# Optimization experiments

Measured on AMD Instinct MI355X. Metric: run time of the kernel, lower is better.

Reference implementation:

```python
import jax, jax.numpy as jnp
import numpy as np
from jax import lax

B, CIN, H, W = 16, 96, 112, 112
C1, C2 = CIN * 2, CIN * 4          # 192, 384 (t1=(2,2))
SQ = 24                            # make_divisible(96//4, 4)
EPS = 1e-5


def _conv(x, w, stride, pad, groups):
    return lax.conv_general_dilated(
        x, w, window_strides=stride, padding=pad,
        feature_group_count=groups,
        dimension_numbers=("NCHW", "OIHW", "NCHW"))


def _bn(x, g, b, m, v):
    scale = (g / jnp.sqrt(v + EPS))[None, :, None, None]
    return (x - m[None, :, None, None]) * scale + b[None, :, None, None]


def _shuffle(x, groups):
    b, c, h, w = x.shape
    return x.reshape(b, groups, c // groups, h, w).transpose(0, 2, 1, 3, 4).reshape(b, c, h, w)


# DYShiftMax channel permutation for g=1: rotate channels left by 1
_DY_IDX = np.roll(np.arange(CIN), -1)


def setup_inputs() -> dict:
    key = jax.random.key(0)
    ks = jax.random.split(key, 16)
    f32 = jnp.float32
    d = {}
    d["x"] = jax.random.normal(ks[0], (B, CIN, H, W), f32)
    # depthwise (k,1) conv, groups=CIN, multiplier 2
    d["w_dw1"] = jax.random.normal(ks[1], (C1, 1, 3, 1), f32) * 0.2
    d["bn1_g"] = jax.random.uniform(ks[2], (C1,), f32, 0.5, 1.5)
    d["bn1_b"] = jax.random.normal(ks[3], (C1,), f32) * 0.1
    d["bn1_m"] = jax.random.normal(ks[4], (C1,), f32) * 0.1
    d["bn1_v"] = jax.random.uniform(ks[5], (C1,), f32, 0.5, 1.5)
    # depthwise (1,k) conv, groups=C1, multiplier 2
    d["w_dw2"] = jax.random.normal(ks[6], (C2, 1, 1, 3), f32) * 0.2
    d["bn2_g"] = jax.random.uniform(ks[7], (C2,), f32, 0.5, 1.5)
    d["bn2_b"] = jax.random.normal(ks[8], (C2,), f32) * 0.1
    d["bn2_m"] = jax.random.normal(ks[9], (C2,), f32) * 0.1
    d["bn2_v"] = jax.random.uniform(ks[10], (C2,), f32, 0.5, 1.5)
    # 1x1 pointwise conv 384 -> 96 (ConvModule, bias-free conv + BN, identity act)
    d["w_pw"] = jax.random.normal(ks[11], (CIN, C2, 1, 1), f32) * (1.0 / np.sqrt(C2))
    d["bn3_g"] = jax.random.uniform(ks[12], (CIN,), f32, 0.5, 1.5)
    d["bn3_b"] = jax.random.normal(ks[13], (CIN,), f32) * 0.1
    d["bn3_m"] = jax.random.normal(ks[14], (CIN,), f32) * 0.1
    d["bn3_v"] = jax.random.uniform(ks[15], (CIN,), f32, 0.5, 1.5)
    # DYShiftMax squeeze-excite FC: CIN -> SQ -> 2*CIN (exp=2)
    k2 = jax.random.split(jax.random.fold_in(key, 1), 4)
    d["fc1_w"] = jax.random.normal(k2[0], (SQ, CIN), f32) * (1.0 / np.sqrt(CIN))
    d["fc1_b"] = jax.random.normal(k2[1], (SQ,), f32) * 0.1
    d["fc2_w"] = jax.random.normal(k2[2], (2 * CIN, SQ), f32) * (1.0 / np.sqrt(SQ))
    d["fc2_b"] = jax.random.normal(k2[3], (2 * CIN,), f32) * 0.1
    return d


def reference(x, w_dw1, bn1_g, bn1_b, bn1_m, bn1_v,
              w_dw2, bn2_g, bn2_b, bn2_m, bn2_v,
              w_pw, bn3_g, bn3_b, bn3_m, bn3_v,
              fc1_w, fc1_b, fc2_w, fc2_b):
    # DepthSpatialSepConv: depthwise (3,1) then depthwise (1,3), each + BN
    h = _conv(x, w_dw1, (1, 1), ((1, 1), (0, 0)), groups=CIN)
    h = _bn(h, bn1_g, bn1_b, bn1_m, bn1_v)
    h = _conv(h, w_dw2, (1, 1), ((0, 0), (1, 1)), groups=C1)
    h = _bn(h, bn2_g, bn2_b, bn2_m, bn2_v)
    # ReLU6 (y2 == 0)
    h = jnp.clip(h, 0.0, 6.0)
    # ChannelShuffle(6)
    h = _shuffle(h, 6)
    # 1x1 ConvModule (groups=1, identity activation) + BN
    h = _conv(h, w_pw, (1, 1), ((0, 0), (0, 0)), groups=1)
    h = _bn(h, bn3_g, bn3_b, bn3_m, bn3_v)
    # DYShiftMax(out, out, (1,0), (0,0), act_relu=False -> exp=2, g=1)
    y = h.mean(axis=(2, 3))                       # [B, CIN] global avg pool
    y = jnp.maximum(y @ fc1_w.T + fc1_b, 0.0)     # Linear + ReLU
    y = y @ fc2_w.T + fc2_b                       # Linear -> [B, 2*CIN]
    y = jnp.clip(y + 3.0, 0.0, 6.0) / 6.0         # HSigmoid
    y = (y - 0.5) * 4.0
    a1 = y[:, :CIN] + 1.0                         # init_a[0] = 1.0
    b1 = y[:, CIN:]                               # init_b[0] = 0.0
    h2 = h[:, _DY_IDX, :, :]                      # shifted channels
    h = h * a1[:, :, None, None] + h2 * b1[:, :, None, None]
    # ChannelShuffle(g2=1) is identity; ChannelShuffle(out//2)
    h = _shuffle(h, CIN // 2)
    # residual (stride==1 and in==out)
    return h + x
```

## Files before the change

### kernel.cpp

```cpp
#include <hip/hip_runtime.h>
#include <hip/hip_bf16.h>

#define BATCH 16
#define CINC 96
#define HGT 112
#define WID 112
#define HW 12544
#define C1N 192
#define C2N 384
#define EPSV 1e-5f

typedef _Float16 f16x8 __attribute__((ext_vector_type(8)));
typedef _Float16 f16x4 __attribute__((ext_vector_type(4)));
typedef float    f32x4 __attribute__((ext_vector_type(4)));

#define WS_S      0
#define WS_A1B1   1536
#define WS_W1F    4608
#define WS_B1F    5184
#define WS_W2F    5376
#define WS_B2F    6528
#define WS_S3     6912
#define WS_B3     7008
#define WS_WPF_BYTES (7104*4)
#define WS_H_BYTES   (WS_WPF_BYTES + CINC*C2N*2)

__global__ void k_prep(const float* __restrict__ wdw1, const float* __restrict__ g1,
                       const float* __restrict__ bb1, const float* __restrict__ m1,
                       const float* __restrict__ v1,
                       const float* __restrict__ wdw2, const float* __restrict__ g2,
                       const float* __restrict__ bb2, const float* __restrict__ m2,
                       const float* __restrict__ v2,
                       const float* __restrict__ wpw, const float* __restrict__ g3,
                       const float* __restrict__ bb3, const float* __restrict__ m3,
                       const float* __restrict__ v3,
                       float* ws)
{
    int t = blockIdx.x * blockDim.x + threadIdx.x;
    int stride = gridDim.x * blockDim.x;
    float* w1f = ws + WS_W1F; float* b1f = ws + WS_B1F;
    float* w2f = ws + WS_W2F; float* b2f = ws + WS_B2F;
    float* s3  = ws + WS_S3;  float* b3f = ws + WS_B3;
    _Float16* wpf = (_Float16*)((char*)ws + WS_WPF_BYTES);

    for (int c = t; c < C1N; c += stride) {
        float s = g1[c] / sqrtf(v1[c] + EPSV);
        w1f[c*3+0] = wdw1[c*3+0] * s;
        w1f[c*3+1] = wdw1[c*3+1] * s;
        w1f[c*3+2] = wdw1[c*3+2] * s;
        b1f[c] = bb1[c] - m1[c] * s;
    }
    for (int c = t; c < C2N; c += stride) {
        float s = g2[c] / sqrtf(v2[c] + EPSV);
        w2f[c*3+0] = wdw2[c*3+0] * s;
        w2f[c*3+1] = wdw2[c*3+1] * s;
        w2f[c*3+2] = wdw2[c*3+2] * s;
        b2f[c] = bb2[c] - m2[c] * s;
    }
    for (int c = t; c < CINC; c += stride) {
        float s = g3[c] / sqrtf(v3[c] + EPSV);
        s3[c] = s; b3f[c] = bb3[c] - m3[c] * s;
    }
    for (int idx = t; idx < CINC * C2N; idx += stride) {
        int e = idx & 7;
        int l2 = idx >> 3;
        int lane = l2 & 63;
        int l3 = l2 >> 6;
        int rt = l3 % 6, ksg = l3 / 6;
        int m = rt * 16 + (lane & 15);
        int k = ksg * 32 + (lane >> 4) * 8 + e;
        int o = (k & 63) * 6 + (k >> 6);
        wpf[idx] = (_Float16)wpw[m * C2N + o];
    }
}

struct PairX {
    f32x4 T[2], M[2], B[2];
    float eT[2], eM[2], eB[2];
};

__global__ __launch_bounds__(256, 2) void k_main8(const float* __restrict__ x,
                                                  const float* __restrict__ ws,
                                                  float* __restrict__ sums,
                                                  _Float16* __restrict__ h_out)
{
    __shared__ __align__(16) char u_raw[256 * 208];
    __shared__ __align__(16) f16x8 wpf_s[1152];
    __shared__ float ssum[CINC];

    int t   = threadIdx.x;
    int bid = blockIdx.x;
    int logical = (bid & 7) * 112 + (bid >> 3);
    int b   = logical / 56;
    int rem = logical - b * 56;
    int y0  = (rem >> 1) * 4;
    int x0  = (rem & 1) * 48;

    int wv = t >> 6, lane = t & 63;
    int r = lane >> 4, c4 = lane & 15;
    int gy = y0 + r;
    int gc = x0 + 4 * c4;
    int col16 = c4, g = r;

    const float* w1f = ws + WS_W1F; const float* b1f = ws + WS_B1F;
    const float* w2f = ws + WS_W2F; const float* b2f = ws + WS_B2F;

    if (t < CINC) ssum[t] = 0.f;

    bool ymok = gy >= 1;
    bool ypok = gy + 1 < HGT;
    bool isE  = (c4 == 0) | (c4 == 15);
    int  ecol = (c4 == 0) ? (x0 - 1) : (x0 + 64);
    bool ev   = isE && ((unsigned)ecol < (unsigned)WID);
    int  secol = ev ? ecol : 0;
    int  tm = ymok ? -WID : 0;
    int  tp = ypok ?  WID : 0;

    f32x4 acc[6][4];
    #pragma unroll
    for (int rt = 0; rt < 6; ++rt)
        #pragma unroll
        for (int ct = 0; ct < 4; ++ct) acc[rt][ct] = (f32x4){0.f, 0.f, 0.f, 0.f};

    const f16x8* wpf_g = (const f16x8*)((const char*)ws + WS_WPF_BYTES);
    long xb = (long)b * CINC * HW;
    const float* xw = x + xb + (long)gy * WID;

    int rotbase = 3 * r + c4;
    char* ub0 = u_raw + (r * 64 + 4 * c4) * 208;

    f16x8 nw0 = wpf_g[t];
    f16x8 nw1 = wpf_g[256 + t];
    f16x8 nw2 = wpf_g[512 + t];
    f16x8 nw3 = wpf_g[768 + t];
    f16x8 nw4 = nw0;
    if (t < 128) nw4 = wpf_g[1024 + t];

    #define LOADCH(dst, q, cuq) {                                         \
        const float* p_ = xw + (long)(cuq) * HW;                          \
        (dst).M[q] = *(const f32x4*)(p_ + gc);                            \
        (dst).T[q] = *(const f32x4*)(p_ + gc + tm);                       \
        (dst).B[q] = *(const f32x4*)(p_ + gc + tp);                       \
        if (isE) {                                                        \
            const float* e_ = p_ + secol;                                 \
            (dst).eM[q] = e_[0]; (dst).eT[q] = e_[tm]; (dst).eB[q] = e_[tp]; \
        } }

    for (int chunk = 0; chunk < 4; ++chunk) {
        if (chunk) __syncthreads();

        wpf_s[t] = nw0;
        wpf_s[256 + t] = nw1;
        wpf_s[512 + t] = nw2;
        wpf_s[768 + t] = nw3;
        if (t < 128) wpf_s[1024 + t] = nw4;

        int cbase = chunk * 24 + wv * 6;
        PairX A, B;
        LOADCH(A, 0, cbase + 0)
        LOADCH(A, 1, cbase + 1)

        #pragma unroll
        for (int p = 0; p < 3; ++p) {
            if (p == 0) { LOADCH(B, 0, cbase + 2) LOADCH(B, 1, cbase + 3) }
            if (p == 1) { LOADCH(A, 0, cbase + 4) LOADCH(A, 1, cbase + 5) }
            PairX& C = (p == 1) ? B : A;

            f16x4 uv[2][4];
            #pragma unroll
            for (int q = 0; q < 2; ++q) {
                int cu = cbase + 2 * p + q;
                int c1a = cu * 2;
                float wa0 = w1f[c1a*3+0], wa1 = w1f[c1a*3+1], wa2 = w1f[c1a*3+2], ba = b1f[c1a];
                float wb0 = w1f[c1a*3+3], wb1 = w1f[c1a*3+4], wb2 = w1f[c1a*3+5], bb = b1f[c1a+1];

                float va[4], vb[4];
                #pragma unroll
                for (int j = 0; j < 4; ++j) {
                    float tt = ymok ? C.T[q][j] : 0.f;
                    float bt = ypok ? C.B[q][j] : 0.f;
                    va[j] = fmaf(wa0, tt, fmaf(wa1, C.M[q][j], fmaf(wa2, bt, ba)));
                    vb[j] = fmaf(wb0, tt, fmaf(wb1, C.M[q][j], fmaf(wb2, bt, bb)));
                }
                float etS = (ymok && ev) ? C.eT[q] : 0.f;
                float ebS = (ypok && ev) ? C.eB[q] : 0.f;
                float emS = ev ? C.eM[q] : 0.f;
                float vea = ev ? fmaf(wa0, etS, fmaf(wa1, emS, fmaf(wa2, ebS, ba))) : 0.f;
                float veb = ev ? fmaf(wb0, etS, fmaf(wb1, emS, fmaf(wb2, ebS, bb))) : 0.f;

                float vLa = __shfl(va[3], (lane + 63) & 63);
                float vLb = __shfl(vb[3], (lane + 63) & 63);
                float vRa = __shfl(va[0], (lane + 1) & 63);
                float vRb = __shfl(vb[0], (lane + 1) & 63);
                if (c4 == 0)  { vLa = vea; vLb = veb; }
                if (c4 == 15) { vRa = vea; vRb = veb; }

                int c2b = cu * 4;
                float pa[6] = {vLa, va[0], va[1], va[2], va[3], vRa};
                float pb[6] = {vLb, vb[0], vb[1], vb[2], vb[3], vRb};
                #pragma unroll
                for (int j = 0; j < 4; ++j) {
                    #pragma unroll
                    for (int jj = 0; jj < 4; ++jj) {
                        float p0 = (jj < 2) ? pa[j]     : pb[j];
                        float p1 = (jj < 2) ? pa[j + 1] : pb[j + 1];
                        float p2 = (jj < 2) ? pa[j + 2] : pb[j + 2];
                        float tv = fmaf(w2f[(c2b+jj)*3+0], p0,
                                   fmaf(w2f[(c2b+jj)*3+1], p1,
                                   fmaf(w2f[(c2b+jj)*3+2], p2, b2f[c2b+jj])));
                        uv[q][j][jj] = (_Float16)fminf(fmaxf(tv, 0.f), 6.f);
                    }
                }
            }
            int slot = (wv * 3 + p + rotbase) % 12;
            char* ubase = ub0 + slot * 16;
            #pragma unroll
            for (int j = 0; j < 4; ++j) {
                f16x8 w = __builtin_shufflevector(uv[0][j], uv[1][j], 0, 1, 2, 3, 4, 5, 6, 7);
                *(f16x8*)(ubase + j * 208) = w;
            }
        }

        if (chunk < 3) {
            int cb = (chunk + 1) * 1152;
            nw0 = wpf_g[cb + t];
            nw1 = wpf_g[cb + 256 + t];
            nw2 = wpf_g[cb + 512 + t];
            nw3 = wpf_g[cb + 768 + t];
            if (t < 128) nw4 = wpf_g[cb + 1024 + t];
        }
        __syncthreads();

        #pragma unroll
        for (int ks = 0; ks < 3; ++ks) {
            f16x8 bfr[4];
            #pragma unroll
            for (int ct = 0; ct < 4; ++ct) {
                int pos = wv * 64 + ct * 16 + col16;
                int sl = (ks * 4 + g + 3 * wv + ((pos >> 2) & 15)) % 12;
                bfr[ct] = *(const f16x8*)(u_raw + pos * 208 + sl * 16);
            }
            #pragma unroll
            for (int rt = 0; rt < 6; ++rt) {
                f16x8 afr = wpf_s[(ks * 6 + rt) * 64 + lane];
                #pragma unroll
                for (int ct = 0; ct < 4; ++ct)
                    acc[rt][ct] = __builtin_amdgcn_mfma_f32_16x16x32_f16(afr, bfr[ct], acc[rt][ct], 0, 0, 0);
            }
        }
    }
    __syncthreads();

    _Float16* h_s = (_Float16*)u_raw;
    const float* s3  = ws + WS_S3;
    const float* b3f = ws + WS_B3;
    #pragma unroll
    for (int rt = 0; rt < 6; ++rt) {
        #pragma unroll
        for (int ct = 0; ct < 4; ++ct) {
            int p = wv * 64 + ct * 16 + col16;
            #pragma unroll
            for (int rr = 0; rr < 4; ++rr) {
                int m = rt * 16 + g * 4 + rr;
                h_s[m * 264 + p] = (_Float16)fmaf(acc[rt][ct][rr], s3[m], b3f[m]);
            }
        }
    }
    __syncthreads();

    #pragma unroll
    for (int i = 0; i < 12; ++i) {
        int flat = i * 2048 + t * 8;
        int m = flat >> 8;
        int p = flat & 255;
        f16x8 hv = *(const f16x8*)(h_s + m * 264 + p);
        int row = y0 + (p >> 6);
        int colg = x0 + (p & 63);
        *(f16x8*)(h_out + ((long)(b * CINC + m)) * HW + (long)row * WID + colg) = hv;

        float s = 0.f;
        if (!(x0 == 48 && (p & 63) < 16)) {
            #pragma unroll
            for (int e = 0; e < 8; ++e) s += (float)hv[e];
        }
        s += __shfl_xor(s, 1);
        s += __shfl_xor(s, 2);
        s += __shfl_xor(s, 4);
        s += __shfl_xor(s, 8);
        s += __shfl_xor(s, 16);
        if ((lane & 31) == 0) atomicAdd(&ssum[m], s);
    }
    __syncthreads();
    if (t < CINC) atomicAdd(&sums[b * CINC + t], ssum[t]);
}

__global__ __launch_bounds__(192) void k_gates(const float* __restrict__ sums,
                                               const float* __restrict__ fc1w,
                                               const float* __restrict__ fc1b,
                                               const float* __restrict__ fc2w,
                                               const float* __restrict__ fc2b,
                                               float* __restrict__ a1b1)
{
    __shared__ float mean_s[CINC];
    __shared__ float mid[24];
    int b = blockIdx.x;
    int t = threadIdx.x;

    if (t < CINC) mean_s[t] = sums[b * CINC + t] * (1.0f / 12544.0f);
    __syncthreads();
    if (t < 24) {
        float d = fc1b[t];
        #pragma unroll 4
        for (int c = 0; c < CINC; ++c) d = fmaf(fc1w[t * CINC + c], mean_s[c], d);
        mid[t] = fmaxf(d, 0.f);
    }
    __syncthreads();
    {
        float d = fc2b[t];
        #pragma unroll
        for (int j = 0; j < 24; ++j) d = fmaf(fc2w[t * 24 + j], mid[j], d);
        float y = fminf(fmaxf(d + 3.f, 0.f), 6.f) * (1.f / 6.f);
        y = (y - 0.5f) * 4.f;
        a1b1[b * 192 + t] = (t < CINC) ? (y + 1.f) : y;
    }
}

__global__ __launch_bounds__(256) void k_final(const _Float16* __restrict__ h,
                                               const float* __restrict__ xin,
                                               const float* __restrict__ a1b1,
                                               float* __restrict__ out)
{
    int q = blockIdx.x * 256 + threadIdx.x;
    int pos4 = q % 3136;
    int bo = q / 3136;
    int o = bo % CINC, b = bo / CINC;
    int c = (o % 48) * 2 + (o / 48);
    int cn = (c + 1) % CINC;

    float av = a1b1[b * 192 + c];
    float bv = a1b1[b * 192 + 96 + c];

    long hb = (long)b * CINC * HW;
    f16x4 hv4 = *(const f16x4*)(h + hb + (long)c  * HW + pos4 * 4);
    f16x4 h2v = *(const f16x4*)(h + hb + (long)cn * HW + pos4 * 4);

    long xo = ((long)(b * CINC + o)) * HW + pos4 * 4;
    f32x4 xv = *(const f32x4*)(xin + xo);
    f32x4 rr;
    #pragma unroll
    for (int j = 0; j < 4; ++j)
        rr[j] = fmaf((float)hv4[j], av, fmaf((float)h2v[j], bv, xv[j]));
    *(f32x4*)(out + xo) = rr;
}

extern "C" void kernel_launch(void* const* d_in, const int* in_sizes, int n_in,
                              void* d_out, int out_size, void* d_ws, size_t ws_size,
                              hipStream_t stream)
{
    const float* x    = (const float*)d_in[0];
    const float* wdw1 = (const float*)d_in[1];
    const float* g1   = (const float*)d_in[2];
    const float* b1   = (const float*)d_in[3];
    const float* m1   = (const float*)d_in[4];
    const float* v1   = (const float*)d_in[5];
    const float* wdw2 = (const float*)d_in[6];
    const float* g2   = (const float*)d_in[7];
    const float* b2   = (const float*)d_in[8];
    const float* m2   = (const float*)d_in[9];
    const float* v2   = (const float*)d_in[10];
    const float* wpw  = (const float*)d_in[11];
    const float* g3   = (const float*)d_in[12];
    const float* b3   = (const float*)d_in[13];
    const float* m3   = (const float*)d_in[14];
    const float* v3   = (const float*)d_in[15];
    const float* fc1w = (const float*)d_in[16];
    const float* fc1b = (const float*)d_in[17];
    const float* fc2w = (const float*)d_in[18];
    const float* fc2b = (const float*)d_in[19];

    float* ws   = (float*)d_ws;
    float* sums = ws + WS_S;
    float* a1b1 = ws + WS_A1B1;
    _Float16* hbuf = (_Float16*)((char*)d_ws + WS_H_BYTES);
    float* out  = (float*)d_out;

    hipMemsetAsync(sums, 0, 1536 * sizeof(float), stream);
    k_prep<<<dim3(40), dim3(256), 0, stream>>>(
        wdw1, g1, b1, m1, v1, wdw2, g2, b2, m2, v2,
        wpw, g3, b3, m3, v3, ws);
    k_main8<<<dim3(896), dim3(256), 0, stream>>>(x, ws, sums, hbuf);
    k_gates<<<dim3(BATCH), dim3(192), 0, stream>>>(sums, fc1w, fc1b, fc2w, fc2b, a1b1);
    k_final<<<dim3(4816896 / 256), dim3(256), 0, stream>>>(hbuf, x, a1b1, out);
}
```

Baseline: 119.2 us.

## Shrink LDS footprint with smaller K-chunks to fit three blocks per CU

Splits the 384-channel reduction into 6 chunks of 64 instead of 4 chunks of 96. This cuts the staged activation and weight tiles to one 48KB shared buffer, and launch bounds move to 3 blocks per CU. Input loads are now prefetched across chunk boundaries. The epilogue writes out the 96 output channels in two passes of 48 so the result fits in the smaller buffer. The goal is higher occupancy to hide memory latency, at the cost of more barriers and tighter register limits that could cause spills.

```diff
diff --git a/kernel.cpp b/kernel.cpp
--- a/kernel.cpp
+++ b/kernel.cpp
@@ -79,13 +79,12 @@
     float eT[2], eM[2], eB[2];
 };
 
-__global__ __launch_bounds__(256, 2) void k_main8(const float* __restrict__ x,
+__global__ __launch_bounds__(256, 3) void k_main9(const float* __restrict__ x,
                                                   const float* __restrict__ ws,
                                                   float* __restrict__ sums,
                                                   _Float16* __restrict__ h_out)
 {
-    __shared__ __align__(16) char u_raw[256 * 208];
-    __shared__ __align__(16) f16x8 wpf_s[1152];
+    __shared__ __align__(16) char smem[49152];
     __shared__ float ssum[CINC];
 
     int t   = threadIdx.x;
@@ -122,19 +121,17 @@
         #pragma unroll
         for (int ct = 0; ct < 4; ++ct) acc[rt][ct] = (f32x4){0.f, 0.f, 0.f, 0.f};
 
+    f16x8* wpf_s = (f16x8*)(smem + 36864);
     const f16x8* wpf_g = (const f16x8*)((const char*)ws + WS_WPF_BYTES);
     long xb = (long)b * CINC * HW;
     const float* xw = x + xb + (long)gy * WID;
 
     int rotbase = 3 * r + c4;
-    char* ub0 = u_raw + (r * 64 + 4 * c4) * 208;
+    char* ub0 = smem + (r * 64 + 4 * c4) * 144;
 
     f16x8 nw0 = wpf_g[t];
     f16x8 nw1 = wpf_g[256 + t];
     f16x8 nw2 = wpf_g[512 + t];
-    f16x8 nw3 = wpf_g[768 + t];
-    f16x8 nw4 = nw0;
-    if (t < 128) nw4 = wpf_g[1024 + t];
 
     #define LOADCH(dst, q, cuq) {                                         \
         const float* p_ = xw + (long)(cuq) * HW;                          \
@@ -146,24 +143,26 @@
             (dst).eM[q] = e_[0]; (dst).eT[q] = e_[tm]; (dst).eB[q] = e_[tp]; \
         } }
 
-    for (int chunk = 0; chunk < 4; ++chunk) {
+    PairX A, B;
+    LOADCH(A, 0, wv * 4 + 0)
+    LOADCH(A, 1, wv * 4 + 1)
+
+    for (int chunk = 0; chunk < 6; ++chunk) {
         if (chunk) __syncthreads();
 
         wpf_s[t] = nw0;
         wpf_s[256 + t] = nw1;
         wpf_s[512 + t] = nw2;
-        wpf_s[768 + t] = nw3;
-        if (t < 128) wpf_s[1024 + t] = nw4;
-
-        int cbase = chunk * 24 + wv * 6;
-        PairX A, B;
-        LOADCH(A, 0, cbase + 0)
-        LOADCH(A, 1, cbase + 1)
-
-        #pragma unroll
-        for (int p = 0; p < 3; ++p) {
+
+        int cbase = chunk * 16 + wv * 4;
+
+        #pragma unroll
+        for (int p = 0; p < 2; ++p) {
             if (p == 0) { LOADCH(B, 0, cbase + 2) LOADCH(B, 1, cbase + 3) }
-            if (p == 1) { LOADCH(A, 0, cbase + 4) LOADCH(A, 1, cbase + 5) }
+            else if (chunk < 5) {
+                LOADCH(A, 0, cbase + 16)
+                LOADCH(A, 1, cbase + 17)
+            }
             PairX& C = (p == 1) ? B : A;
 
             f16x4 uv[2][4];
@@ -212,33 +211,32 @@
                     }
                 }
             }
-            int slot = (wv * 3 + p + rotbase) % 12;
+            int slot = (wv * 2 + p + rotbase) % 9;
             char* ubase = ub0 + slot * 16;
             #pragma unroll
             for (int j = 0; j < 4; ++j) {
                 f16x8 w = __builtin_shufflevector(uv[0][j], uv[1][j], 0, 1, 2, 3, 4, 5, 6, 7);
-                *(f16x8*)(ubase + j * 208) = w;
-            }
-        }
-
-        if (chunk < 3) {
-            int cb = (chunk + 1) * 1152;
+                *(f16x8*)(ubase + j * 144) = w;
+            }
+        }
+
+        if (chunk < 5) {
+            int cb = (chunk + 1) * 768;
             nw0 = wpf_g[cb + t];
             nw1 = wpf_g[cb + 256 + t];
             nw2 = wpf_g[cb + 512 + t];
-            nw3 = wpf_g[cb + 768 + t];
-            if (t < 128) nw4 = wpf_g[cb + 1024 + t];
         }
         __syncthreads();
 
         #pragma unroll
-        for (int ks = 0; ks < 3; ++ks) {
+        for (int ks = 0; ks < 2; ++ks) {
             f16x8 bfr[4];
             #pragma unroll
             for (int ct = 0; ct < 4; ++ct) {
                 int pos = wv * 64 + ct * 16 + col16;
-                int sl = (ks * 4 + g + 3 * wv + ((pos >> 2) & 15)) % 12;
-                bfr[ct] = *(const f16x8*)(u_raw + pos * 208 + sl * 16);
+                int rb = 3 * (pos >> 6) + ((pos & 63) >> 2);
+                int sl = (ks * 4 + g + rb) % 9;
+                bfr[ct] = *(const f16x8*)(smem + pos * 144 + sl * 16);
             }
             #pragma unroll
             for (int rt = 0; rt < 6; ++rt) {
@@ -251,46 +249,51 @@
     }
     __syncthreads();
 
-    _Float16* h_s = (_Float16*)u_raw;
+    _Float16* h_s = (_Float16*)smem;
     const float* s3  = ws + WS_S3;
     const float* b3f = ws + WS_B3;
     #pragma unroll
-    for (int rt = 0; rt < 6; ++rt) {
-        #pragma unroll
-        for (int ct = 0; ct < 4; ++ct) {
-            int p = wv * 64 + ct * 16 + col16;
-            #pragma unroll
-            for (int rr = 0; rr < 4; ++rr) {
-                int m = rt * 16 + g * 4 + rr;
-                h_s[m * 264 + p] = (_Float16)fmaf(acc[rt][ct][rr], s3[m], b3f[m]);
-            }
-        }
-    }
-    __syncthreads();
-
-    #pragma unroll
-    for (int i = 0; i < 12; ++i) {
-        int flat = i * 2048 + t * 8;
-        int m = flat >> 8;
-        int p = flat & 255;
-        f16x8 hv = *(const f16x8*)(h_s + m * 264 + p);
-        int row = y0 + (p >> 6);
-        int colg = x0 + (p & 63);
-        *(f16x8*)(h_out + ((long)(b * CINC + m)) * HW + (long)row * WID + colg) = hv;
-
-        float s = 0.f;
-        if (!(x0 == 48 && (p & 63) < 16)) {
-            #pragma unroll
-            for (int e = 0; e < 8; ++e) s += (float)hv[e];
-        }
-        s += __shfl_xor(s, 1);
-        s += __shfl_xor(s, 2);
-        s += __shfl_xor(s, 4);
-        s += __shfl_xor(s, 8);
-        s += __shfl_xor(s, 16);
-        if ((lane & 31) == 0) atomicAdd(&ssum[m], s);
-    }
-    __syncthreads();
+    for (int pass = 0; pass < 2; ++pass) {
+        #pragma unroll
+        for (int rt3 = 0; rt3 < 3; ++rt3) {
+            int rt = pass * 3 + rt3;
+            #pragma unroll
+            for (int ct = 0; ct < 4; ++ct) {
+                int p = wv * 64 + ct * 16 + col16;
+                #pragma unroll
+                for (int rr = 0; rr < 4; ++rr) {
+                    int m = rt * 16 + g * 4 + rr;
+                    h_s[(rt3 * 16 + g * 4 + rr) * 264 + p] =
+                        (_Float16)fmaf(acc[rt][ct][rr], s3[m], b3f[m]);
+                }
+            }
+        }
+        __syncthreads();
+        #pragma unroll
+        for (int i = 0; i < 6; ++i) {
+            int flat = i * 2048 + t * 8;
+            int mL = flat >> 8;
+            int p = flat & 255;
+            f16x8 hv = *(const f16x8*)(h_s + mL * 264 + p);
+            int m = pass * 48 + mL;
+            int row = y0 + (p >> 6);
+            int colg = x0 + (p & 63);
+            *(f16x8*)(h_out + ((long)(b * CINC + m)) * HW + (long)row * WID + colg) = hv;
+
+            float s = 0.f;
+            if (!(x0 == 48 && (p & 63) < 16)) {
+                #pragma unroll
+                for (int e = 0; e < 8; ++e) s += (float)hv[e];
+            }
+            s += __shfl_xor(s, 1);
+            s += __shfl_xor(s, 2);
+            s += __shfl_xor(s, 4);
+            s += __shfl_xor(s, 8);
+            s += __shfl_xor(s, 16);
+            if ((lane & 31) == 0) atomicAdd(&ssum[m], s);
+        }
+        __syncthreads();
+    }
     if (t < CINC) atomicAdd(&sums[b * CINC + t], ssum[t]);
 }
 
@@ -388,7 +391,7 @@
     k_prep<<<dim3(40), dim3(256), 0, stream>>>(
         wdw1, g1, b1, m1, v1, wdw2, g2, b2, m2, v2,
         wpw, g3, b3, m3, v3, ws);
-    k_main8<<<dim3(896), dim3(256), 0, stream>>>(x, ws, sums, hbuf);
+    k_main9<<<dim3(896), dim3(256), 0, stream>>>(x, ws, sums, hbuf);
     k_gates<<<dim3(BATCH), dim3(192), 0, stream>>>(sums, fc1w, fc1b, fc2w, fc2b, a1b1);
     k_final<<<dim3(4816896 / 256), dim3(256), 0, stream>>>(hbuf, x, a1b1, out);
 }
```

Measured after the change: 391.1 us. 3.28x slower.
